# Kernel tuning notes

Measured on AMD Instinct MI355X. Metric: run time of the kernel, lower is better.

The kernel has to match this reference:

```python
import jax, jax.numpy as jnp
import numpy as np

N_CLASSES = 64  # number of initial (labeled) classes


def _compute_logits_radii(h, protos, radii):
    """Complex-valued radii logits.
    h: [B,N,2,D] (real/imag), protos: [B,2,C,D], radii: [B,C].
    dist[b,n,c] = sum_d (hr-pr)^2 + (hi-pi)^2 (matches _compute_distances_complex).
    logits = -dist / (2*radii)  (standard IMP radii-logit form).
    Expanded as |h|^2 + |p|^2 - 2 h.p so the cross term is a GEMM (no [N,C,D] tensor).
    """
    hr, hi = h[:, :, 0, :], h[:, :, 1, :]          # [B,N,D]
    pr, pi = protos[:, 0], protos[:, 1]            # [B,C,D]
    h_sq = jnp.sum(hr * hr + hi * hi, axis=-1)     # [B,N]
    p_sq = jnp.sum(pr * pr + pi * pi, axis=-1)     # [B,C]
    cross = jnp.einsum('bnd,bcd->bnc', hr, pr) + jnp.einsum('bnd,bcd->bnc', hi, pi)
    dist = h_sq[:, :, None] + p_sq[:, None, :] - 2.0 * cross   # [B,N,C]
    return -dist / (2.0 * radii[:, None, :])


def setup_inputs() -> dict:
    key = jax.random.key(0)
    k1, k2, k3, k4, k5 = jax.random.split(key, 5)
    B, N, C, D = 1, 8192, 512, 512
    h = jax.random.normal(k1, (B, N, 2, D), dtype=jnp.float32)
    protos = jax.random.normal(k2, (B, 2, C, D), dtype=jnp.float32)
    # radii must be positive (it divides the distance); keep away from 0
    radii = jax.random.uniform(k3, (B, C), dtype=jnp.float32) * 0.9 + 0.1
    y = jax.random.randint(k4, (N,), 0, N_CLASSES)
    support_labels = jax.random.randint(k5, (C,), 0, N_CLASSES)
    return {"h": h, "protos": protos, "radii": radii, "y": y,
            "support_labels": support_labels, "n_initial_clusters": N_CLASSES}


def reference(h, protos, radii, y, support_labels, n_initial_clusters):
    logits = _compute_logits_radii(h, protos, radii)[0]          # [N,C], B=1 squeeze
    labels = jnp.where(y >= n_initial_clusters, -1, y)           # [N]
    support_targets = labels[:, None] == support_labels[None, :]  # [N,C] bool

    neg_inf = jnp.asarray(-jnp.inf, logits.dtype)
    # best prototype among the query's own class ('or' target)
    target_logits = jnp.where(support_targets, logits, neg_inf)
    best_targets = jnp.argmax(target_logits, axis=1)             # [N]

    # vectorized per-class best prototype: weights[n,c]=1 iff c is the argmax
    # of logits[n,:] restricted to clusters whose label == support_labels[c]
    max_per_class = jax.ops.segment_max(logits.T, support_labels,
                                        num_segments=N_CLASSES)  # [K,N]
    weights = (logits == max_per_class[support_labels, :].T).astype(logits.dtype)  # [N,C]

    # weighted cross entropy at the 'or' target
    log_probs = jax.nn.log_softmax(logits, axis=1)
    nll = -jnp.take_along_axis(log_probs, best_targets[:, None], axis=1)[:, 0]
    w = jnp.take_along_axis(weights, best_targets[:, None], axis=1)[:, 0]
    loss = jnp.mean(nll * w)

    # accuracy: predicted cluster -> its class label
    support_preds = jnp.argmax(logits, axis=1)
    y_pred = support_labels[support_preds]
    acc_val = jnp.sum((y_pred == labels).astype(jnp.float32))
    return loss, acc_val
```

## Files before the change

### kernel.cpp

```cpp
#include <hip/hip_runtime.h>
#include <stdint.h>

typedef unsigned short u16;
typedef __attribute__((ext_vector_type(8))) short shortx8;
typedef __attribute__((ext_vector_type(4))) float floatx4;

#define N_ROWS 8192
#define N_COLS 512
#define KDIM   1024

__device__ __forceinline__ u16 f2bf(float f) {
    union { float f; uint32_t u; } x; x.f = f;
    uint32_t u = x.u;
    uint32_t r = (u + 0x7FFFu + ((u >> 16) & 1u)) >> 16;
    return (u16)r;
}

__device__ __forceinline__ void async_copy16(const void* g, void* l) {
    __builtin_amdgcn_global_load_lds(
        (const __attribute__((address_space(1))) void*)g,
        (__attribute__((address_space(3))) void*)l, 16, 0, 0);
}

__global__ __launch_bounds__(256) void conv_hp(const float* __restrict__ h,
                                               const float* __restrict__ protos,
                                               u16* __restrict__ hb,
                                               u16* __restrict__ bb,
                                               float* __restrict__ hsq,
                                               float* __restrict__ psq) {
    int t = threadIdx.x, lane = t & 63, w = t >> 6;
    int bid = blockIdx.x;
    if (bid < 512) {
        int wave = bid * 4 + w;
        for (int q = 0; q < 4; q++) {
            int row = wave * 4 + q;
            const float4* src = (const float4*)(h + (size_t)row * KDIM);
            ushort4* dst = (ushort4*)(hb + (size_t)row * KDIM);
            float s = 0.0f;
            #pragma unroll
            for (int j = 0; j < 4; j++) {
                float4 v = src[lane + j * 64];
                s += v.x * v.x + v.y * v.y + v.z * v.z + v.w * v.w;
                dst[lane + j * 64] = make_ushort4(f2bf(v.x), f2bf(v.y), f2bf(v.z), f2bf(v.w));
            }
            #pragma unroll
            for (int off = 32; off; off >>= 1) s += __shfl_xor(s, off);
            if (lane == 0) hsq[row] = s;
        }
    } else {
        int c = (bid - 512) * 4 + w;
        const float4* pr = (const float4*)(protos + (size_t)c * 512);
        const float4* pi = (const float4*)(protos + 512 * 512 + (size_t)c * 512);
        ushort4* dr = (ushort4*)(bb + (size_t)c * KDIM);
        ushort4* di = (ushort4*)(bb + (size_t)c * KDIM + 512);
        float s = 0.0f;
        #pragma unroll
        for (int j = 0; j < 2; j++) {
            float4 a = pr[lane + j * 64];
            float4 b = pi[lane + j * 64];
            s += a.x * a.x + a.y * a.y + a.z * a.z + a.w * a.w;
            s += b.x * b.x + b.y * b.y + b.z * b.z + b.w * b.w;
            dr[lane + j * 64] = make_ushort4(f2bf(a.x), f2bf(a.y), f2bf(a.z), f2bf(a.w));
            di[lane + j * 64] = make_ushort4(f2bf(b.x), f2bf(b.y), f2bf(b.z), f2bf(b.w));
        }
        #pragma unroll
        for (int off = 32; off; off >>= 1) s += __shfl_xor(s, off);
        if (lane == 0) psq[c] = s;
    }
}

__global__ __launch_bounds__(256) void gemm_partials(const u16* __restrict__ hb,
                                                     const u16* __restrict__ bb,
                                                     const float* __restrict__ hsq,
                                                     const float* __restrict__ psq,
                                                     const float* __restrict__ radii,
                                                     const int* __restrict__ y,
                                                     const int* __restrict__ slab,
                                                     const int* __restrict__ ninit_p,
                                                     float* __restrict__ pmax_g,
                                                     int* __restrict__ pidx_g,
                                                     float* __restrict__ prmax_g,
                                                     float* __restrict__ pc0_g,
                                                     float* __restrict__ psum_g,
                                                     float* __restrict__ l0arr) {
    constexpr int BM = 128, BN = 64, BK = 64;
    __shared__ __align__(16) u16 As[BM * BK];
    __shared__ __align__(16) u16 Bs[BN * BK];
    __shared__ float smax[2][128];
    __shared__ int   scol[2][128];
    __shared__ float srmx[2][128];
    __shared__ float sc0v[2][128];
    __shared__ float ssum[2][128];

    int t = threadIdx.x, lane = t & 63, w = t >> 6;
    int wr = (w & 1) * 64;
    int wc = (w >> 1) * 32;
    int bm0 = blockIdx.x * BM;
    int bn0 = blockIdx.y * BN;

    int tr = t >> 3, tc = t & 7;
    const u16* gA[4]; u16* lA[4];
    #pragma unroll
    for (int i = 0; i < 4; i++) {
        int row = tr + 32 * i;
        int kc = tc ^ (row & 7);
        gA[i] = hb + (size_t)(bm0 + row) * KDIM + kc * 8;
        lA[i] = &As[(t + 256 * i) * 8];
    }
    const u16* gB[2]; u16* lB[2];
    #pragma unroll
    for (int i = 0; i < 2; i++) {
        int row = tr + 32 * i;
        int kc = tc ^ (row & 7);
        gB[i] = bb + (size_t)(bn0 + row) * KDIM + kc * 8;
        lB[i] = &Bs[(t + 256 * i) * 8];
    }

    floatx4 acc[4][2] = {};

    int kq = lane >> 4, l7 = lane & 7, m = lane & 15;
    int swz0 = ((kq) ^ l7) * 8;
    int swz1 = ((4 + kq) ^ l7) * 8;
    const u16* paA = &As[(wr + m) * BK];
    const u16* paB = &Bs[(wc + m) * BK];

    for (int k0 = 0; k0 < KDIM; k0 += BK) {
        __syncthreads();
        #pragma unroll
        for (int i = 0; i < 4; i++) async_copy16(gA[i], lA[i]);
        #pragma unroll
        for (int i = 0; i < 2; i++) async_copy16(gB[i], lB[i]);
        #pragma unroll
        for (int i = 0; i < 4; i++) gA[i] += BK;
        #pragma unroll
        for (int i = 0; i < 2; i++) gB[i] += BK;
        __syncthreads();

        #pragma unroll
        for (int s = 0; s < 2; s++) {
            int sw = s ? swz1 : swz0;
            shortx8 af[4], bf[2];
            #pragma unroll
            for (int i = 0; i < 4; i++) af[i] = *(const shortx8*)(paA + i * 16 * BK + sw);
            #pragma unroll
            for (int j = 0; j < 2; j++) bf[j] = *(const shortx8*)(paB + j * 16 * BK + sw);
            #pragma unroll
            for (int i = 0; i < 4; i++)
                #pragma unroll
                for (int j = 0; j < 2; j++)
                    acc[i][j] = __builtin_amdgcn_mfma_f32_16x16x32_bf16(af[i], bf[j], acc[i][j], 0, 0, 0);
        }
    }

    int c0 = bn0 + wc + m, c1 = c0 + 16;
    float ps0 = psq[c0], ps1 = psq[c1];
    float inv0 = 0.5f / radii[c0], inv1 = 0.5f / radii[c1];
    int sl0 = slab[c0], sl1 = slab[c1];
    int slabz = slab[0];
    int ninit = ninit_p[0];
    int ch = w >> 1;
    bool isL0 = (bn0 == 0) && (wc == 0) && (m == 0);

    #pragma unroll
    for (int i = 0; i < 4; i++) {
        #pragma unroll
        for (int r = 0; r < 4; r++) {
            int n = bm0 + wr + i * 16 + kq * 4 + r;
            float hsqn = hsq[n];
            int yv = y[n];
            int lab = (yv >= ninit) ? -1 : yv;
            float v0 = (2.0f * acc[i][0][r] - hsqn - ps0) * inv0;
            float v1 = (2.0f * acc[i][1][r] - hsqn - ps1) * inv1;
            if (isL0) l0arr[n] = v0;

            float bmax = v0; int bcol = c0;
            if (v1 > bmax) { bmax = v1; bcol = c1; }
            float brm = -INFINITY;
            if (sl0 == lab) brm = v0;
            if (sl1 == lab && v1 > brm) brm = v1;
            float bc0 = -INFINITY;
            if (sl0 == slabz) bc0 = v0;
            if (sl1 == slabz && v1 > bc0) bc0 = v1;
            #pragma unroll
            for (int off = 1; off < 16; off <<= 1) {
                float ov = __shfl_xor(bmax, off); int oc = __shfl_xor(bcol, off);
                if (ov > bmax || (ov == bmax && oc < bcol)) { bmax = ov; bcol = oc; }
                float orv = __shfl_xor(brm, off); if (orv > brm) brm = orv;
                float oc0 = __shfl_xor(bc0, off); if (oc0 > bc0) bc0 = oc0;
            }
            float se = __expf(v0 - bmax) + __expf(v1 - bmax);
            #pragma unroll
            for (int off = 1; off < 16; off <<= 1) se += __shfl_xor(se, off);
            if (m == 0) {
                int rl = (w & 1) * 64 + i * 16 + kq * 4 + r;
                smax[ch][rl] = bmax; scol[ch][rl] = bcol;
                srmx[ch][rl] = brm;  sc0v[ch][rl] = bc0; ssum[ch][rl] = se;
            }
        }
    }
    __syncthreads();
    if (t < 128) {
        int n = bm0 + t;
        size_t gi_ = (size_t)blockIdx.y * N_ROWS + n;
        float m0 = smax[0][t], m1 = smax[1][t];
        int i0 = scol[0][t], i1 = scol[1][t];
        float gm; int gi;
        if (m0 > m1 || (m0 == m1 && i0 < i1)) { gm = m0; gi = i0; }
        else { gm = m1; gi = i1; }
        pmax_g[gi_] = gm;
        pidx_g[gi_] = gi;
        prmax_g[gi_] = fmaxf(srmx[0][t], srmx[1][t]);
        pc0_g[gi_]  = fmaxf(sc0v[0][t], sc0v[1][t]);
        psum_g[gi_] = ssum[0][t] * __expf(m0 - gm) + ssum[1][t] * __expf(m1 - gm);
    }
}

__global__ __launch_bounds__(256) void combine(const float* __restrict__ pmax_g,
                                               const int* __restrict__ pidx_g,
                                               const float* __restrict__ prmax_g,
                                               const float* __restrict__ pc0_g,
                                               const float* __restrict__ psum_g,
                                               const float* __restrict__ l0arr,
                                               const int* __restrict__ y,
                                               const int* __restrict__ slab,
                                               const int* __restrict__ ninit_p,
                                               float* __restrict__ out) {
    int t = threadIdx.x, lane = t & 63, w = t >> 6;
    int n = blockIdx.x * 256 + t;

    float gm = -INFINITY; int gi = 0x7fffffff;
    float rm = -INFINITY, c0m = -INFINITY;
    float pm[8];
    #pragma unroll
    for (int cb = 0; cb < 8; cb++) {
        size_t idx = (size_t)cb * N_ROWS + n;
        float p = pmax_g[idx]; int pi = pidx_g[idx];
        pm[cb] = p;
        if (p > gm || (p == gm && pi < gi)) { gm = p; gi = pi; }
        rm = fmaxf(rm, prmax_g[idx]);
        c0m = fmaxf(c0m, pc0_g[idx]);
    }
    float den = 0.0f;
    #pragma unroll
    for (int cb = 0; cb < 8; cb++)
        den += psum_g[(size_t)cb * N_ROWS + n] * __expf(pm[cb] - gm);
    float lse = gm + __logf(den);

    int yv = y[n];
    int lab = (yv >= ninit_p[0]) ? -1 : yv;
    float nll, wgt;
    if (rm != -INFINITY) { nll = lse - rm; wgt = 1.0f; }
    else {
        float l0 = l0arr[n];
        nll = lse - l0;
        wgt = (l0 == c0m) ? 1.0f : 0.0f;
    }
    int ypred = slab[gi];
    float li = nll * wgt * (1.0f / (float)N_ROWS);
    float ai = (ypred == lab) ? 1.0f : 0.0f;

    #pragma unroll
    for (int off = 32; off; off >>= 1) {
        li += __shfl_xor(li, off);
        ai += __shfl_xor(ai, off);
    }
    __shared__ float pl[4], pa_[4];
    if (lane == 0) { pl[w] = li; pa_[w] = ai; }
    __syncthreads();
    if (t == 0) {
        atomicAdd(&out[0], pl[0] + pl[1] + pl[2] + pl[3]);
        atomicAdd(&out[1], pa_[0] + pa_[1] + pa_[2] + pa_[3]);
    }
}

extern "C" void kernel_launch(void* const* d_in, const int* in_sizes, int n_in,
                              void* d_out, int out_size, void* d_ws, size_t ws_size,
                              hipStream_t stream) {
    const float* h      = (const float*)d_in[0];
    const float* protos = (const float*)d_in[1];
    const float* radii  = (const float*)d_in[2];
    const int*   y      = (const int*)d_in[3];
    const int*   slab   = (const int*)d_in[4];
    const int*   ninit  = (const int*)d_in[5];
    float* out = (float*)d_out;

    char* ws = (char*)d_ws;
    u16*   hb    = (u16*)(ws);
    u16*   bb    = (u16*)(ws + 16777216);
    float* hsq   = (float*)(ws + 17825792);
    float* psq   = (float*)(ws + 17858560);
    float* pmax  = (float*)(ws + 17860608);
    int*   pidx  = (int*)  (ws + 18122752);
    float* prmax = (float*)(ws + 18384896);
    float* pc0   = (float*)(ws + 18647040);
    float* psum  = (float*)(ws + 18909184);
    float* l0arr = (float*)(ws + 19171328);

    hipMemsetAsync(d_out, 0, 2 * sizeof(float), stream);

    conv_hp<<<640, 256, 0, stream>>>(h, protos, hb, bb, hsq, psq);
    dim3 g(N_ROWS / 128, N_COLS / 64);
    gemm_partials<<<g, 256, 0, stream>>>(hb, bb, hsq, psq, radii, y, slab, ninit,
                                         pmax, pidx, prmax, pc0, psum, l0arr);
    combine<<<N_ROWS / 256, 256, 0, stream>>>(pmax, pidx, prmax, pc0, psum,
                                              l0arr, y, slab, ninit, out);
}
```

Baseline: 117.4 us.

## Double-buffer GEMM LDS tiles, widen N tile to 128, fold output zeroing into conversion

The GEMM kernel now uses two LDS buffers per operand, so the async global-to-LDS loads for the next K step are issued while MFMAs run on the current buffer. This replaces the old load-then-wait pattern. The block tile grows from 128x64 to 128x128, giving 4x4 accumulators per wave. That halves the column-block count, so the combine kernel reduces 4 partials instead of 8. The hipMemsetAsync of the output is replaced by a write inside the conversion kernel, saving one launch. The trade-off is a grid of only 256 blocks with 64KB LDS each, which means low occupancy per CU.

```diff
diff --git a/kernel.cpp b/kernel.cpp
--- a/kernel.cpp
+++ b/kernel.cpp
@@ -27,9 +27,11 @@
                                                u16* __restrict__ hb,
                                                u16* __restrict__ bb,
                                                float* __restrict__ hsq,
-                                               float* __restrict__ psq) {
+                                               float* __restrict__ psq,
+                                               float* __restrict__ out) {
     int t = threadIdx.x, lane = t & 63, w = t >> 6;
     int bid = blockIdx.x;
+    if (bid == 639 && t < 2) out[t] = 0.0f;
     if (bid < 512) {
         int wave = bid * 4 + w;
         for (int q = 0; q < 4; q++) {
@@ -83,9 +85,9 @@
                                                      float* __restrict__ pc0_g,
                                                      float* __restrict__ psum_g,
                                                      float* __restrict__ l0arr) {
-    constexpr int BM = 128, BN = 64, BK = 64;
-    __shared__ __align__(16) u16 As[BM * BK];
-    __shared__ __align__(16) u16 Bs[BN * BK];
+    constexpr int BM = 128, BN = 128, BK = 64;
+    __shared__ __align__(16) u16 As[2][BM * BK];
+    __shared__ __align__(16) u16 Bs[2][BN * BK];
     __shared__ float smax[2][128];
     __shared__ int   scol[2][128];
     __shared__ float srmx[2][128];
@@ -94,68 +96,73 @@
 
     int t = threadIdx.x, lane = t & 63, w = t >> 6;
     int wr = (w & 1) * 64;
-    int wc = (w >> 1) * 32;
+    int wc = (w >> 1) * 64;
     int bm0 = blockIdx.x * BM;
     int bn0 = blockIdx.y * BN;
 
     int tr = t >> 3, tc = t & 7;
-    const u16* gA[4]; u16* lA[4];
+    const u16* gA[4]; const u16* gB[4]; int lo[4];
     #pragma unroll
     for (int i = 0; i < 4; i++) {
         int row = tr + 32 * i;
         int kc = tc ^ (row & 7);
         gA[i] = hb + (size_t)(bm0 + row) * KDIM + kc * 8;
-        lA[i] = &As[(t + 256 * i) * 8];
-    }
-    const u16* gB[2]; u16* lB[2];
-    #pragma unroll
-    for (int i = 0; i < 2; i++) {
-        int row = tr + 32 * i;
-        int kc = tc ^ (row & 7);
         gB[i] = bb + (size_t)(bn0 + row) * KDIM + kc * 8;
-        lB[i] = &Bs[(t + 256 * i) * 8];
-    }
-
-    floatx4 acc[4][2] = {};
+        lo[i] = (t + 256 * i) * 8;
+    }
+
+    floatx4 acc[4][4] = {};
 
     int kq = lane >> 4, l7 = lane & 7, m = lane & 15;
     int swz0 = ((kq) ^ l7) * 8;
     int swz1 = ((4 + kq) ^ l7) * 8;
-    const u16* paA = &As[(wr + m) * BK];
-    const u16* paB = &Bs[(wc + m) * BK];
-
+
+    #pragma unroll
+    for (int i = 0; i < 4; i++) {
+        async_copy16(gA[i], &As[0][lo[i]]);
+        async_copy16(gB[i], &Bs[0][lo[i]]);
+        gA[i] += BK; gB[i] += BK;
+    }
+
+    int buf = 0;
     for (int k0 = 0; k0 < KDIM; k0 += BK) {
         __syncthreads();
-        #pragma unroll
-        for (int i = 0; i < 4; i++) async_copy16(gA[i], lA[i]);
-        #pragma unroll
-        for (int i = 0; i < 2; i++) async_copy16(gB[i], lB[i]);
-        #pragma unroll
-        for (int i = 0; i < 4; i++) gA[i] += BK;
-        #pragma unroll
-        for (int i = 0; i < 2; i++) gB[i] += BK;
-        __syncthreads();
-
+        if (k0 + BK < KDIM) {
+            int nb = buf ^ 1;
+            #pragma unroll
+            for (int i = 0; i < 4; i++) {
+                async_copy16(gA[i], &As[nb][lo[i]]);
+                async_copy16(gB[i], &Bs[nb][lo[i]]);
+                gA[i] += BK; gB[i] += BK;
+            }
+        }
+        const u16* pa = &As[buf][(wr + m) * BK];
+        const u16* pb = &Bs[buf][(wc + m) * BK];
         #pragma unroll
         for (int s = 0; s < 2; s++) {
             int sw = s ? swz1 : swz0;
-            shortx8 af[4], bf[2];
-            #pragma unroll
-            for (int i = 0; i < 4; i++) af[i] = *(const shortx8*)(paA + i * 16 * BK + sw);
-            #pragma unroll
-            for (int j = 0; j < 2; j++) bf[j] = *(const shortx8*)(paB + j * 16 * BK + sw);
+            shortx8 af[4], bf[4];
+            #pragma unroll
+            for (int i = 0; i < 4; i++) af[i] = *(const shortx8*)(pa + i * 16 * BK + sw);
+            #pragma unroll
+            for (int j = 0; j < 4; j++) bf[j] = *(const shortx8*)(pb + j * 16 * BK + sw);
             #pragma unroll
             for (int i = 0; i < 4; i++)
                 #pragma unroll
-                for (int j = 0; j < 2; j++)
+                for (int j = 0; j < 4; j++)
                     acc[i][j] = __builtin_amdgcn_mfma_f32_16x16x32_bf16(af[i], bf[j], acc[i][j], 0, 0, 0);
         }
-    }
-
-    int c0 = bn0 + wc + m, c1 = c0 + 16;
-    float ps0 = psq[c0], ps1 = psq[c1];
-    float inv0 = 0.5f / radii[c0], inv1 = 0.5f / radii[c1];
-    int sl0 = slab[c0], sl1 = slab[c1];
+        buf ^= 1;
+    }
+
+    int c_[4]; float ps_[4], inv_[4]; int sl_[4];
+    #pragma unroll
+    for (int j = 0; j < 4; j++) {
+        c_[j] = bn0 + wc + j * 16 + m;
+        ps_[j] = psq[c_[j]];
+        inv_[j] = 0.5f / radii[c_[j]];
+        sl_[j] = slab[c_[j]];
+    }
     int slabz = slab[0];
     int ninit = ninit_p[0];
     int ch = w >> 1;
@@ -169,18 +176,20 @@
             float hsqn = hsq[n];
             int yv = y[n];
             int lab = (yv >= ninit) ? -1 : yv;
-            float v0 = (2.0f * acc[i][0][r] - hsqn - ps0) * inv0;
-            float v1 = (2.0f * acc[i][1][r] - hsqn - ps1) * inv1;
-            if (isL0) l0arr[n] = v0;
-
-            float bmax = v0; int bcol = c0;
-            if (v1 > bmax) { bmax = v1; bcol = c1; }
-            float brm = -INFINITY;
-            if (sl0 == lab) brm = v0;
-            if (sl1 == lab && v1 > brm) brm = v1;
-            float bc0 = -INFINITY;
-            if (sl0 == slabz) bc0 = v0;
-            if (sl1 == slabz && v1 > bc0) bc0 = v1;
+            float v[4];
+            #pragma unroll
+            for (int j = 0; j < 4; j++)
+                v[j] = (2.0f * acc[i][j][r] - hsqn - ps_[j]) * inv_[j];
+            if (isL0) l0arr[n] = v[0];
+
+            float bmax = v[0]; int bcol = c_[0];
+            float brm = -INFINITY, bc0 = -INFINITY;
+            #pragma unroll
+            for (int j = 0; j < 4; j++) {
+                if (v[j] > bmax) { bmax = v[j]; bcol = c_[j]; }
+                if (sl_[j] == lab   && v[j] > brm) brm = v[j];
+                if (sl_[j] == slabz && v[j] > bc0) bc0 = v[j];
+            }
             #pragma unroll
             for (int off = 1; off < 16; off <<= 1) {
                 float ov = __shfl_xor(bmax, off); int oc = __shfl_xor(bcol, off);
@@ -188,7 +197,9 @@
                 float orv = __shfl_xor(brm, off); if (orv > brm) brm = orv;
                 float oc0 = __shfl_xor(bc0, off); if (oc0 > bc0) bc0 = oc0;
             }
-            float se = __expf(v0 - bmax) + __expf(v1 - bmax);
+            float se = 0.0f;
+            #pragma unroll
+            for (int j = 0; j < 4; j++) se += __expf(v[j] - bmax);
             #pragma unroll
             for (int off = 1; off < 16; off <<= 1) se += __shfl_xor(se, off);
             if (m == 0) {
@@ -230,9 +241,9 @@
 
     float gm = -INFINITY; int gi = 0x7fffffff;
     float rm = -INFINITY, c0m = -INFINITY;
-    float pm[8];
-    #pragma unroll
-    for (int cb = 0; cb < 8; cb++) {
+    float pm[4];
+    #pragma unroll
+    for (int cb = 0; cb < 4; cb++) {
         size_t idx = (size_t)cb * N_ROWS + n;
         float p = pmax_g[idx]; int pi = pidx_g[idx];
         pm[cb] = p;
@@ -242,7 +253,7 @@
     }
     float den = 0.0f;
     #pragma unroll
-    for (int cb = 0; cb < 8; cb++)
+    for (int cb = 0; cb < 4; cb++)
         den += psum_g[(size_t)cb * N_ROWS + n] * __expf(pm[cb] - gm);
     float lse = gm + __logf(den);
 
@@ -296,10 +307,8 @@
     float* psum  = (float*)(ws + 18909184);
     float* l0arr = (float*)(ws + 19171328);
 
-    hipMemsetAsync(d_out, 0, 2 * sizeof(float), stream);
-
-    conv_hp<<<640, 256, 0, stream>>>(h, protos, hb, bb, hsq, psq);
-    dim3 g(N_ROWS / 128, N_COLS / 64);
+    conv_hp<<<640, 256, 0, stream>>>(h, protos, hb, bb, hsq, psq, out);
+    dim3 g(N_ROWS / 128, N_COLS / 128);
     gemm_partials<<<g, 256, 0, stream>>>(hb, bb, hsq, psq, radii, y, slab, ninit,
                                          pmax, pidx, prmax, pc0, psum, l0arr);
     combine<<<N_ROWS / 256, 256, 0, stream>>>(pmax, pidx, prmax, pc0, psum,
```

Result: no change. 118.0 us (+0.6%).

## Fuse combine pass into GEMM via last-block counter and drop memset

Applied to the files above, without the earlier changes.

Removes the separate combine kernel: each GEMM block bumps a per-row-tile counter, and the last of the eight column blocks for a row tile reduces the partial results and accumulates loss and accuracy. Zeroing of the output and counters moves into the conversion kernel, so the hipMemsetAsync goes away. This cuts one kernel launch and a memset from the stream. In exchange it adds a threadfence and an atomic per block, plus a serialized tail in the last blocks.

```diff
diff --git a/kernel.cpp b/kernel.cpp
--- a/kernel.cpp
+++ b/kernel.cpp
@@ -27,9 +27,15 @@
                                                u16* __restrict__ hb,
                                                u16* __restrict__ bb,
                                                float* __restrict__ hsq,
-                                               float* __restrict__ psq) {
+                                               float* __restrict__ psq,
+                                               float* __restrict__ out,
+                                               int* __restrict__ cnt) {
     int t = threadIdx.x, lane = t & 63, w = t >> 6;
     int bid = blockIdx.x;
+    if (bid == 639) {
+        if (t < 2) out[t] = 0.0f;
+        if (t < 64) cnt[t] = 0;
+    }
     if (bid < 512) {
         int wave = bid * 4 + w;
         for (int q = 0; q < 4; q++) {
@@ -82,7 +88,9 @@
                                                      float* __restrict__ prmax_g,
                                                      float* __restrict__ pc0_g,
                                                      float* __restrict__ psum_g,
-                                                     float* __restrict__ l0arr) {
+                                                     float* __restrict__ l0arr,
+                                                     int* __restrict__ cnt,
+                                                     float* __restrict__ out) {
     constexpr int BM = 128, BN = 64, BK = 64;
     __shared__ __align__(16) u16 As[BM * BK];
     __shared__ __align__(16) u16 Bs[BN * BK];
@@ -213,63 +221,60 @@
         pc0_g[gi_]  = fmaxf(sc0v[0][t], sc0v[1][t]);
         psum_g[gi_] = ssum[0][t] * __expf(m0 - gm) + ssum[1][t] * __expf(m1 - gm);
     }
-}
-
-__global__ __launch_bounds__(256) void combine(const float* __restrict__ pmax_g,
-                                               const int* __restrict__ pidx_g,
-                                               const float* __restrict__ prmax_g,
-                                               const float* __restrict__ pc0_g,
-                                               const float* __restrict__ psum_g,
-                                               const float* __restrict__ l0arr,
-                                               const int* __restrict__ y,
-                                               const int* __restrict__ slab,
-                                               const int* __restrict__ ninit_p,
-                                               float* __restrict__ out) {
-    int t = threadIdx.x, lane = t & 63, w = t >> 6;
-    int n = blockIdx.x * 256 + t;
-
-    float gm = -INFINITY; int gi = 0x7fffffff;
-    float rm = -INFINITY, c0m = -INFINITY;
-    float pm[8];
-    #pragma unroll
-    for (int cb = 0; cb < 8; cb++) {
-        size_t idx = (size_t)cb * N_ROWS + n;
-        float p = pmax_g[idx]; int pi = pidx_g[idx];
-        pm[cb] = p;
-        if (p > gm || (p == gm && pi < gi)) { gm = p; gi = pi; }
-        rm = fmaxf(rm, prmax_g[idx]);
-        c0m = fmaxf(c0m, pc0_g[idx]);
-    }
-    float den = 0.0f;
-    #pragma unroll
-    for (int cb = 0; cb < 8; cb++)
-        den += psum_g[(size_t)cb * N_ROWS + n] * __expf(pm[cb] - gm);
-    float lse = gm + __logf(den);
-
-    int yv = y[n];
-    int lab = (yv >= ninit_p[0]) ? -1 : yv;
-    float nll, wgt;
-    if (rm != -INFINITY) { nll = lse - rm; wgt = 1.0f; }
-    else {
-        float l0 = l0arr[n];
-        nll = lse - l0;
-        wgt = (l0 == c0m) ? 1.0f : 0.0f;
-    }
-    int ypred = slab[gi];
-    float li = nll * wgt * (1.0f / (float)N_ROWS);
-    float ai = (ypred == lab) ? 1.0f : 0.0f;
-
-    #pragma unroll
-    for (int off = 32; off; off >>= 1) {
-        li += __shfl_xor(li, off);
-        ai += __shfl_xor(ai, off);
-    }
-    __shared__ float pl[4], pa_[4];
-    if (lane == 0) { pl[w] = li; pa_[w] = ai; }
+
     __syncthreads();
-    if (t == 0) {
-        atomicAdd(&out[0], pl[0] + pl[1] + pl[2] + pl[3]);
-        atomicAdd(&out[1], pa_[0] + pa_[1] + pa_[2] + pa_[3]);
+    __threadfence();
+    __shared__ int lastFlag;
+    if (t == 0) lastFlag = (atomicAdd(&cnt[blockIdx.x], 1) == 7) ? 1 : 0;
+    __syncthreads();
+    if (lastFlag) {
+        __threadfence();
+        float li = 0.0f, ai = 0.0f;
+        if (t < 128) {
+            int n = bm0 + t;
+            float gm = -INFINITY; int gi = 0x7fffffff;
+            float rm = -INFINITY, c0m = -INFINITY;
+            float pm[8];
+            #pragma unroll
+            for (int cb = 0; cb < 8; cb++) {
+                size_t idx = (size_t)cb * N_ROWS + n;
+                float p = pmax_g[idx]; int pi = pidx_g[idx];
+                pm[cb] = p;
+                if (p > gm || (p == gm && pi < gi)) { gm = p; gi = pi; }
+                rm = fmaxf(rm, prmax_g[idx]);
+                c0m = fmaxf(c0m, pc0_g[idx]);
+            }
+            float den = 0.0f;
+            #pragma unroll
+            for (int cb = 0; cb < 8; cb++)
+                den += psum_g[(size_t)cb * N_ROWS + n] * __expf(pm[cb] - gm);
+            float lse = gm + __logf(den);
+
+            int yv = y[n];
+            int lab = (yv >= ninit) ? -1 : yv;
+            float nll, wgt;
+            if (rm != -INFINITY) { nll = lse - rm; wgt = 1.0f; }
+            else {
+                float l0 = l0arr[n];
+                nll = lse - l0;
+                wgt = (l0 == c0m) ? 1.0f : 0.0f;
+            }
+            int ypred = slab[gi];
+            li = nll * wgt * (1.0f / (float)N_ROWS);
+            ai = (ypred == lab) ? 1.0f : 0.0f;
+        }
+        #pragma unroll
+        for (int off = 32; off; off >>= 1) {
+            li += __shfl_xor(li, off);
+            ai += __shfl_xor(ai, off);
+        }
+        __shared__ float pl[4], pa_[4];
+        if (lane == 0) { pl[w] = li; pa_[w] = ai; }
+        __syncthreads();
+        if (t == 0) {
+            atomicAdd(&out[0], pl[0] + pl[1] + pl[2] + pl[3]);
+            atomicAdd(&out[1], pa_[0] + pa_[1] + pa_[2] + pa_[3]);
+        }
     }
 }
 
@@ -295,13 +300,11 @@
     float* pc0   = (float*)(ws + 18647040);
     float* psum  = (float*)(ws + 18909184);
     float* l0arr = (float*)(ws + 19171328);
-
-    hipMemsetAsync(d_out, 0, 2 * sizeof(float), stream);
-
-    conv_hp<<<640, 256, 0, stream>>>(h, protos, hb, bb, hsq, psq);
+    int*   cnt   = (int*)  (ws + 19204096);
+
+    conv_hp<<<640, 256, 0, stream>>>(h, protos, hb, bb, hsq, psq, out, cnt);
     dim3 g(N_ROWS / 128, N_COLS / 64);
     gemm_partials<<<g, 256, 0, stream>>>(hb, bb, hsq, psq, radii, y, slab, ninit,
-                                         pmax, pidx, prmax, pc0, psum, l0arr);
-    combine<<<N_ROWS / 256, 256, 0, stream>>>(pmax, pidx, prmax, pc0, psum,
-                                              l0arr, y, slab, ninit, out);
-}
+                                         pmax, pidx, prmax, pc0, psum, l0arr,
+                                         cnt, out);
+}
```

New measurement: 155.3 us. +32.3%, slower.

## Double-buffer GEMM LDS tiles and fold output zeroing into conversion kernel

Applied to the files above, without the earlier changes.

The GEMM kernel now keeps two LDS buffers for the A and B tiles. It issues the async global-to-LDS copies for the next K tile before computing on the current one, so each iteration has one barrier instead of two and the loads overlap the MFMA work. The separate hipMemsetAsync of the two-float output is removed; one thread pair in the conversion kernel zeroes it instead, saving a launch. LDS use doubles, which could lower occupancy.

```diff
diff --git a/kernel.cpp b/kernel.cpp
--- a/kernel.cpp
+++ b/kernel.cpp
@@ -27,9 +27,11 @@
                                                u16* __restrict__ hb,
                                                u16* __restrict__ bb,
                                                float* __restrict__ hsq,
-                                               float* __restrict__ psq) {
+                                               float* __restrict__ psq,
+                                               float* __restrict__ out) {
     int t = threadIdx.x, lane = t & 63, w = t >> 6;
     int bid = blockIdx.x;
+    if (bid == 639 && t < 2) out[t] = 0.0f;
     if (bid < 512) {
         int wave = bid * 4 + w;
         for (int q = 0; q < 4; q++) {
@@ -84,8 +86,8 @@
                                                      float* __restrict__ psum_g,
                                                      float* __restrict__ l0arr) {
     constexpr int BM = 128, BN = 64, BK = 64;
-    __shared__ __align__(16) u16 As[BM * BK];
-    __shared__ __align__(16) u16 Bs[BN * BK];
+    __shared__ __align__(16) u16 As[2][BM * BK];
+    __shared__ __align__(16) u16 Bs[2][BN * BK];
     __shared__ float smax[2][128];
     __shared__ int   scol[2][128];
     __shared__ float srmx[2][128];
@@ -99,21 +101,21 @@
     int bn0 = blockIdx.y * BN;
 
     int tr = t >> 3, tc = t & 7;
-    const u16* gA[4]; u16* lA[4];
+    const u16* gA[4]; int loA[4];
     #pragma unroll
     for (int i = 0; i < 4; i++) {
         int row = tr + 32 * i;
         int kc = tc ^ (row & 7);
         gA[i] = hb + (size_t)(bm0 + row) * KDIM + kc * 8;
-        lA[i] = &As[(t + 256 * i) * 8];
-    }
-    const u16* gB[2]; u16* lB[2];
+        loA[i] = (t + 256 * i) * 8;
+    }
+    const u16* gB[2]; int loB[2];
     #pragma unroll
     for (int i = 0; i < 2; i++) {
         int row = tr + 32 * i;
         int kc = tc ^ (row & 7);
         gB[i] = bb + (size_t)(bn0 + row) * KDIM + kc * 8;
-        lB[i] = &Bs[(t + 256 * i) * 8];
+        loB[i] = (t + 256 * i) * 8;
     }
 
     floatx4 acc[4][2] = {};
@@ -121,21 +123,24 @@
     int kq = lane >> 4, l7 = lane & 7, m = lane & 15;
     int swz0 = ((kq) ^ l7) * 8;
     int swz1 = ((4 + kq) ^ l7) * 8;
-    const u16* paA = &As[(wr + m) * BK];
-    const u16* paB = &Bs[(wc + m) * BK];
-
+
+    #pragma unroll
+    for (int i = 0; i < 4; i++) { async_copy16(gA[i], &As[0][loA[i]]); gA[i] += BK; }
+    #pragma unroll
+    for (int i = 0; i < 2; i++) { async_copy16(gB[i], &Bs[0][loB[i]]); gB[i] += BK; }
+
+    int buf = 0;
     for (int k0 = 0; k0 < KDIM; k0 += BK) {
         __syncthreads();
-        #pragma unroll
-        for (int i = 0; i < 4; i++) async_copy16(gA[i], lA[i]);
-        #pragma unroll
-        for (int i = 0; i < 2; i++) async_copy16(gB[i], lB[i]);
-        #pragma unroll
-        for (int i = 0; i < 4; i++) gA[i] += BK;
-        #pragma unroll
-        for (int i = 0; i < 2; i++) gB[i] += BK;
-        __syncthreads();
-
+        if (k0 + BK < KDIM) {
+            int nb = buf ^ 1;
+            #pragma unroll
+            for (int i = 0; i < 4; i++) { async_copy16(gA[i], &As[nb][loA[i]]); gA[i] += BK; }
+            #pragma unroll
+            for (int i = 0; i < 2; i++) { async_copy16(gB[i], &Bs[nb][loB[i]]); gB[i] += BK; }
+        }
+        const u16* paA = &As[buf][(wr + m) * BK];
+        const u16* paB = &Bs[buf][(wc + m) * BK];
         #pragma unroll
         for (int s = 0; s < 2; s++) {
             int sw = s ? swz1 : swz0;
@@ -150,6 +155,7 @@
                 for (int j = 0; j < 2; j++)
                     acc[i][j] = __builtin_amdgcn_mfma_f32_16x16x32_bf16(af[i], bf[j], acc[i][j], 0, 0, 0);
         }
+        buf ^= 1;
     }
 
     int c0 = bn0 + wc + m, c1 = c0 + 16;
@@ -296,9 +302,7 @@
     float* psum  = (float*)(ws + 18909184);
     float* l0arr = (float*)(ws + 19171328);
 
-    hipMemsetAsync(d_out, 0, 2 * sizeof(float), stream);
-
-    conv_hp<<<640, 256, 0, stream>>>(h, protos, hb, bb, hsq, psq);
+    conv_hp<<<640, 256, 0, stream>>>(h, protos, hb, bb, hsq, psq, out);
     dim3 g(N_ROWS / 128, N_COLS / 64);
     gemm_partials<<<g, 256, 0, stream>>>(hb, bb, hsq, psq, radii, y, slab, ninit,
                                          pmax, pidx, prmax, pc0, psum, l0arr);
```

Measured after the change: 119.0 us. Within noise of the previous version (+1.4%).
